# Performance work log

Measured on AMD Instinct MI355X. Metric: run time of the kernel, lower is better.

The kernel has to match this reference:

```python
import jax, jax.numpy as jnp
import numpy as np

N_NODES = 100000
N_EDGES = 1600000
IN_DIM = 128
HID_DIM = 128
OUT_DIM = 64
NUM_GRAPHS = 64


def setup_inputs() -> dict:
    key = jax.random.key(0)
    k = jax.random.split(key, 8)
    x = jax.random.normal(k[0], (N_NODES, IN_DIM), dtype=jnp.float32)
    edge_index = jax.random.randint(k[1], (2, N_EDGES), 0, N_NODES, dtype=jnp.int64)
    batch = jnp.sort(jax.random.randint(k[2], (N_NODES,), 0, NUM_GRAPHS, dtype=jnp.int64))
    # glorot-ish init for GCN weights, zero bias (PyG default)
    W1 = jax.random.normal(k[3], (IN_DIM, HID_DIM), dtype=jnp.float32) / np.sqrt(IN_DIM)
    b1 = jnp.zeros((HID_DIM,), dtype=jnp.float32)
    W2 = jax.random.normal(k[4], (HID_DIM, OUT_DIM), dtype=jnp.float32) / np.sqrt(HID_DIM)
    b2 = jnp.zeros((OUT_DIM,), dtype=jnp.float32)
    return {"x": x, "edge_index": edge_index, "batch": batch,
            "W1": W1, "b1": b1, "W2": W2, "b2": b2}


def _gcn_conv(x, W, b, src, dst, norm, n_nodes):
    # x' = scatter_add_{dst}(norm * (xW)[src]) + b   (self-loops already in src/dst)
    h = x @ W                              # [N, D_out]
    msg = norm[:, None] * h[src]           # [E+N, D_out] gather + scale
    out = jax.ops.segment_sum(msg, dst, num_segments=n_nodes)
    return out + b


def _gcn_norm(src, dst, n_nodes):
    # symmetric normalization with self-loops: deg^-1/2[src] * deg^-1/2[dst]
    deg = jax.ops.segment_sum(jnp.ones_like(dst, dtype=jnp.float32), dst,
                              num_segments=n_nodes)
    dinv = jnp.where(deg > 0, jax.lax.rsqrt(deg), 0.0)
    return dinv[src] * dinv[dst]


def reference(x, edge_index, batch, W1, b1, W2, b2):
    n = x.shape[0]
    loops = jnp.arange(n, dtype=edge_index.dtype)
    src = jnp.concatenate([edge_index[0], loops])
    dst = jnp.concatenate([edge_index[1], loops])
    norm = _gcn_norm(src, dst, n)

    h = jax.nn.relu(_gcn_conv(x, W1, b1, src, dst, norm, n))
    h = jax.nn.relu(_gcn_conv(h, W2, b2, src, dst, norm, n))

    # global mean pool per graph
    sums = jax.ops.segment_sum(h, batch, num_segments=NUM_GRAPHS)
    cnts = jax.ops.segment_sum(jnp.ones((n,), dtype=h.dtype), batch,
                               num_segments=NUM_GRAPHS)
    return sums / jnp.maximum(cnts, 1.0)[:, None]
```

## Files before the change

kernel.cpp:

```cpp
#include <hip/hip_runtime.h>

typedef unsigned short ushort_t;
typedef unsigned int uint_t;
typedef __attribute__((ext_vector_type(8))) short bf16x8;
typedef __attribute__((ext_vector_type(4))) float f32x4;

__device__ inline ushort_t bf16_rne(float f) {
    uint_t u = __float_as_uint(f);
    return (ushort_t)((u + 0x7FFFu + ((u >> 16) & 1u)) >> 16);
}

__device__ inline uint_t pack2(float lo, float hi) {
    return (uint_t)bf16_rne(lo) | ((uint_t)bf16_rne(hi) << 16);
}

__device__ inline void acc8(uint4 v, float* a) {
    a[0] += __uint_as_float(v.x << 16);
    a[1] += __uint_as_float(v.x & 0xFFFF0000u);
    a[2] += __uint_as_float(v.y << 16);
    a[3] += __uint_as_float(v.y & 0xFFFF0000u);
    a[4] += __uint_as_float(v.z << 16);
    a[5] += __uint_as_float(v.z & 0xFFFF0000u);
    a[6] += __uint_as_float(v.w << 16);
    a[7] += __uint_as_float(v.w & 0xFFFF0000u);
}

__device__ inline void set8(uint4 v, float* a) {
    a[0] = __uint_as_float(v.x << 16);
    a[1] = __uint_as_float(v.x & 0xFFFF0000u);
    a[2] = __uint_as_float(v.y << 16);
    a[3] = __uint_as_float(v.y & 0xFFFF0000u);
    a[4] = __uint_as_float(v.z << 16);
    a[5] = __uint_as_float(v.z & 0xFFFF0000u);
    a[6] = __uint_as_float(v.w << 16);
    a[7] = __uint_as_float(v.w & 0xFFFF0000u);
}


#define BSH 8
#define NBMAX 512
#define EPB 4096

__global__ __launch_bounds__(256) void k_bhist(const int* __restrict__ dst,
                                               int* __restrict__ bcnt, int E, int nb) {
    __shared__ int h[NBMAX];
    const int tid = threadIdx.x;
    for (int i = tid; i < NBMAX; i += 256) h[i] = 0;
    __syncthreads();
    const int e0 = blockIdx.x * EPB;
    for (int i = tid; i < EPB; i += 256) {
        int e = e0 + i;
        if (e < E) atomicAdd(&h[dst[e] >> BSH], 1);
    }
    __syncthreads();
    for (int i = tid; i < nb; i += 256)
        if (h[i]) atomicAdd(&bcnt[i], h[i]);
}

__global__ __launch_bounds__(512) void k_bscan(const int* __restrict__ bcnt,
                                               int* __restrict__ boff,
                                               int* __restrict__ bcur, int nb) {
    __shared__ int a[NBMAX];
    const int t = threadIdx.x;
    int v = (t < nb) ? bcnt[t] : 0;
    a[t] = v;
    __syncthreads();
    for (int off = 1; off < NBMAX; off <<= 1) {
        int x = (t >= off) ? a[t - off] : 0;
        __syncthreads();
        a[t] += x;
        __syncthreads();
    }
    if (t < nb) {
        int excl = a[t] - v;
        boff[t] = excl;
        bcur[t] = excl;
    }
}

__global__ __launch_bounds__(256) void k_bscatter(const int* __restrict__ src,
                                                  const int* __restrict__ dst,
                                                  int* __restrict__ bcur,
                                                  int2* __restrict__ pairs, int E, int nb) {
    __shared__ int h[NBMAX];
    __shared__ int base[NBMAX];
    const int tid = threadIdx.x;
    for (int i = tid; i < NBMAX; i += 256) h[i] = 0;
    __syncthreads();
    const int e0 = blockIdx.x * EPB;
    for (int i = tid; i < EPB; i += 256) {
        int e = e0 + i;
        if (e < E) atomicAdd(&h[dst[e] >> BSH], 1);
    }
    __syncthreads();
    for (int b = tid; b < nb; b += 256) {
        int c = h[b];
        base[b] = c ? atomicAdd(&bcur[b], c) : 0;
        h[b] = 0;
    }
    __syncthreads();
    for (int i = tid; i < EPB; i += 256) {
        int e = e0 + i;
        if (e < E) {
            int s = src[e], d = dst[e];
            int bk = d >> BSH;
            int off = atomicAdd(&h[bk], 1);
            pairs[base[bk] + off] = make_int2(s, d);
        }
    }
}

__global__ __launch_bounds__(256) void k_bcsr(const int2* __restrict__ pairs,
                                              const int* __restrict__ boff,
                                              const int* __restrict__ bcurEnd,
                                              int* __restrict__ rowptr,
                                              int* __restrict__ rowend,
                                              float* __restrict__ dinv,
                                              int* __restrict__ csr, int n) {
    __shared__ int deg[256], sc[256], cur[256];
    const int t = threadIdx.x;
    const int b = blockIdx.x;
    const int beg = boff[b], end = bcurEnd[b];
    deg[t] = 0;
    __syncthreads();
    for (int i = beg + t; i < end; i += 256) {
        int2 p = pairs[i];
        atomicAdd(&deg[p.y & 255], 1);
    }
    __syncthreads();
    int dv = deg[t];
    sc[t] = dv;
    __syncthreads();
    for (int off = 1; off < 256; off <<= 1) {
        int x = (t >= off) ? sc[t - off] : 0;
        __syncthreads();
        sc[t] += x;
        __syncthreads();
    }
    int excl = sc[t] - dv;
    cur[t] = excl;
    int d = (b << BSH) + t;
    if (d < n) {
        int r = beg + excl;
        rowptr[d] = r;
        rowend[d] = r + dv;
        dinv[d] = rsqrtf((float)dv + 1.0f);
    }
    __syncthreads();
    for (int i = beg + t; i < end; i += 256) {
        int2 p = pairs[i];
        int off = atomicAdd(&cur[p.y & 255], 1);
        csr[beg + off] = p.x;
    }
}


__global__ __launch_bounds__(256) void k_prep_w(const float* __restrict__ W1,
                                                const float* __restrict__ W2,
                                                ushort_t* __restrict__ Wt1,
                                                ushort_t* __restrict__ Wt2) {
    int idx = blockIdx.x * 256 + threadIdx.x;
    if (idx < 16384) {
        int k = idx >> 7, c = idx & 127;
        Wt1[c * 128 + k] = bf16_rne(W1[idx]);
    } else if (idx < 24576) {
        int j = idx - 16384;
        int k = j >> 6, c = j & 63;
        Wt2[c * 128 + k] = bf16_rne(W2[j]);
    }
}


__global__ __launch_bounds__(256) void k_gemm1(const float* __restrict__ X,
                                               const ushort_t* __restrict__ Wt,
                                               const float* __restrict__ dinv,
                                               ushort_t* __restrict__ G, int n) {
    constexpr int KP = 136;
    constexpr int NW = 64, NT = 4;
    __shared__ ushort_t Xs[128 * KP];
    __shared__ ushort_t Ws[128 * KP];

    const int tid = threadIdx.x;
    const int row0 = blockIdx.x * 128;

#pragma unroll
    for (int i = 0; i < 16; i++) {
        int idx = tid * 4 + i * 1024;
        int r = idx >> 7, k = idx & 127;
        int gr = row0 + r;
        float4 v = make_float4(0.f, 0.f, 0.f, 0.f);
        if (gr < n) v = *(const float4*)&X[(size_t)gr * 128 + k];
        ushort4 o;
        o.x = bf16_rne(v.x); o.y = bf16_rne(v.y);
        o.z = bf16_rne(v.z); o.w = bf16_rne(v.w);
        *(ushort4*)&Xs[r * KP + k] = o;
    }
#pragma unroll
    for (int i = 0; i < 8; i++) {
        int idx = tid * 8 + i * 2048;
        int r = idx >> 7, k = idx & 127;
        *(uint4*)&Ws[r * KP + k] = *(const uint4*)&Wt[idx];
    }
    __syncthreads();

    const int lane = tid & 63;
    const int wid = tid >> 6;
    const int wm = wid & 1, wn = wid >> 1;
    const int lr = lane & 15, kg = lane >> 4;

    f32x4 acc[4][NT];
#pragma unroll
    for (int mi = 0; mi < 4; mi++)
#pragma unroll
        for (int ni = 0; ni < NT; ni++)
#pragma unroll
            for (int q = 0; q < 4; q++) acc[mi][ni][q] = 0.f;

    const ushort_t* xb = &Xs[(wm * 64 + lr) * KP + kg * 8];
    const ushort_t* wb = &Ws[(wn * NW + lr) * KP + kg * 8];

#pragma unroll
    for (int ks = 0; ks < 4; ks++) {
        bf16x8 a[4], b[NT];
#pragma unroll
        for (int mi = 0; mi < 4; mi++)
            a[mi] = *(const bf16x8*)&xb[mi * 16 * KP + ks * 32];
#pragma unroll
        for (int ni = 0; ni < NT; ni++)
            b[ni] = *(const bf16x8*)&wb[ni * 16 * KP + ks * 32];
#pragma unroll
        for (int mi = 0; mi < 4; mi++)
#pragma unroll
            for (int ni = 0; ni < NT; ni++)
                acc[mi][ni] = __builtin_amdgcn_mfma_f32_16x16x32_bf16(
                    a[mi], b[ni], acc[mi][ni], 0, 0, 0);
    }

#pragma unroll
    for (int mi = 0; mi < 4; mi++) {
        int r0 = row0 + wm * 64 + mi * 16 + kg * 4;
#pragma unroll
        for (int r = 0; r < 4; r++) {
            int gr = r0 + r;
            if (gr < n) {
                float s = dinv[gr];
#pragma unroll
                for (int ni = 0; ni < NT; ni++) {
                    int c = wn * NW + ni * 16 + lr;
                    G[(size_t)gr * 128 + c] = bf16_rne(s * acc[mi][ni][r]);
                }
            }
        }
    }
}


__global__ __launch_bounds__(256) void k_gather_gemm2(const int* __restrict__ rowptr,
                                                      const int* __restrict__ rowend,
                                                      const int* __restrict__ csr,
                                                      const ushort_t* __restrict__ G1,
                                                      const float* __restrict__ dinv,
                                                      const float* __restrict__ b1,
                                                      const ushort_t* __restrict__ Wt2,
                                                      ushort_t* __restrict__ G2, int n) {
    constexpr int KP = 136;
    __shared__ ushort_t Xs[128 * KP];
    __shared__ ushort_t Ws[64 * KP];

    const int tid = threadIdx.x;
    const int row0 = blockIdx.x * 128;

#pragma unroll
    for (int i = 0; i < 4; i++) {
        int idx = tid * 8 + i * 2048;
        int r = idx >> 7, k = idx & 127;
        *(uint4*)&Ws[r * KP + k] = *(const uint4*)&Wt2[idx];
    }

    const int grp = tid >> 4;
    const int lane = tid & 15;
    const int koff = lane * 8;
    for (int it = 0; it < 8; it++) {
        int r = grp + it * 16;
        int g = row0 + r;
        uint4 ov = make_uint4(0u, 0u, 0u, 0u);
        if (g < n) {
            float a[8];
            set8(*(const uint4*)&G1[(size_t)g * 128 + koff], a);
            int e = rowptr[g];
            const int end = rowend[g];
            for (; e + 3 < end; e += 4) {
                int s0 = csr[e], s1 = csr[e + 1], s2 = csr[e + 2], s3 = csr[e + 3];
                uint4 v0 = *(const uint4*)&G1[(size_t)s0 * 128 + koff];
                uint4 v1 = *(const uint4*)&G1[(size_t)s1 * 128 + koff];
                uint4 v2 = *(const uint4*)&G1[(size_t)s2 * 128 + koff];
                uint4 v3 = *(const uint4*)&G1[(size_t)s3 * 128 + koff];
                acc8(v0, a); acc8(v1, a); acc8(v2, a); acc8(v3, a);
            }
            for (; e < end; e++) {
                int s0 = csr[e];
                acc8(*(const uint4*)&G1[(size_t)s0 * 128 + koff], a);
            }
            const float di = dinv[g];
            float4 bb0 = *(const float4*)&b1[koff];
            float4 bb1 = *(const float4*)&b1[koff + 4];
            ov.x = pack2(fmaxf(di * a[0] + bb0.x, 0.f), fmaxf(di * a[1] + bb0.y, 0.f));
            ov.y = pack2(fmaxf(di * a[2] + bb0.z, 0.f), fmaxf(di * a[3] + bb0.w, 0.f));
            ov.z = pack2(fmaxf(di * a[4] + bb1.x, 0.f), fmaxf(di * a[5] + bb1.y, 0.f));
            ov.w = pack2(fmaxf(di * a[6] + bb1.z, 0.f), fmaxf(di * a[7] + bb1.w, 0.f));
        }
        *(uint4*)&Xs[r * KP + koff] = ov;
    }
    __syncthreads();

    const int lane64 = tid & 63;
    const int wid = tid >> 6;
    const int wm = wid & 1, wn = wid >> 1;
    const int lr = lane64 & 15, kg = lane64 >> 4;

    f32x4 acc[4][2];
#pragma unroll
    for (int mi = 0; mi < 4; mi++)
#pragma unroll
        for (int ni = 0; ni < 2; ni++)
#pragma unroll
            for (int q = 0; q < 4; q++) acc[mi][ni][q] = 0.f;

    const ushort_t* xb = &Xs[(wm * 64 + lr) * KP + kg * 8];
    const ushort_t* wb = &Ws[(wn * 32 + lr) * KP + kg * 8];

#pragma unroll
    for (int ks = 0; ks < 4; ks++) {
        bf16x8 a[4], b[2];
#pragma unroll
        for (int mi = 0; mi < 4; mi++)
            a[mi] = *(const bf16x8*)&xb[mi * 16 * KP + ks * 32];
#pragma unroll
        for (int ni = 0; ni < 2; ni++)
            b[ni] = *(const bf16x8*)&wb[ni * 16 * KP + ks * 32];
#pragma unroll
        for (int mi = 0; mi < 4; mi++)
#pragma unroll
            for (int ni = 0; ni < 2; ni++)
                acc[mi][ni] = __builtin_amdgcn_mfma_f32_16x16x32_bf16(
                    a[mi], b[ni], acc[mi][ni], 0, 0, 0);
    }

#pragma unroll
    for (int mi = 0; mi < 4; mi++) {
        int r0 = row0 + wm * 64 + mi * 16 + kg * 4;
#pragma unroll
        for (int r = 0; r < 4; r++) {
            int gr = r0 + r;
            if (gr < n) {
                float s = dinv[gr];
#pragma unroll
                for (int ni = 0; ni < 2; ni++) {
                    int c = wn * 32 + ni * 16 + lr;
                    G2[(size_t)gr * 64 + c] = bf16_rne(s * acc[mi][ni][r]);
                }
            }
        }
    }
}


__global__ __launch_bounds__(256) void k_gather64_pool(const int* __restrict__ rowptr,
                                                       const int* __restrict__ rowend,
                                                       const int* __restrict__ csr,
                                                       const ushort_t* __restrict__ G,
                                                       const float* __restrict__ dinv,
                                                       const float* __restrict__ b,
                                                       const int* __restrict__ batch,
                                                       float* __restrict__ pool, int n) {
    __shared__ float po[32][72];
    __shared__ int pg[32];
    const int grp = threadIdx.x >> 3;
    const int lane = threadIdx.x & 7;
    const int g = blockIdx.x * 32 + grp;
    const int koff = lane * 8;

    float o8[8] = {0.f, 0.f, 0.f, 0.f, 0.f, 0.f, 0.f, 0.f};
    if (g < n) {
        float a[8];
        set8(*(const uint4*)&G[(size_t)g * 64 + koff], a);
        int e = rowptr[g];
        const int end = rowend[g];
        for (; e + 3 < end; e += 4) {
            int s0 = csr[e], s1 = csr[e + 1], s2 = csr[e + 2], s3 = csr[e + 3];
            uint4 v0 = *(const uint4*)&G[(size_t)s0 * 64 + koff];
            uint4 v1 = *(const uint4*)&G[(size_t)s1 * 64 + koff];
            uint4 v2 = *(const uint4*)&G[(size_t)s2 * 64 + koff];
            uint4 v3 = *(const uint4*)&G[(size_t)s3 * 64 + koff];
            acc8(v0, a); acc8(v1, a); acc8(v2, a); acc8(v3, a);
        }
        for (; e < end; e++) {
            int s0 = csr[e];
            acc8(*(const uint4*)&G[(size_t)s0 * 64 + koff], a);
        }
        const float di = dinv[g];
        float4 bb0 = *(const float4*)&b[koff];
        float4 bb1 = *(const float4*)&b[koff + 4];
        o8[0] = fmaxf(di * a[0] + bb0.x, 0.f);
        o8[1] = fmaxf(di * a[1] + bb0.y, 0.f);
        o8[2] = fmaxf(di * a[2] + bb0.z, 0.f);
        o8[3] = fmaxf(di * a[3] + bb0.w, 0.f);
        o8[4] = fmaxf(di * a[4] + bb1.x, 0.f);
        o8[5] = fmaxf(di * a[5] + bb1.y, 0.f);
        o8[6] = fmaxf(di * a[6] + bb1.z, 0.f);
        o8[7] = fmaxf(di * a[7] + bb1.w, 0.f);
    }
    if (lane == 0) pg[grp] = (g < n) ? batch[g] : -1;
    *(float4*)&po[grp][koff] = make_float4(o8[0], o8[1], o8[2], o8[3]);
    *(float4*)&po[grp][koff + 4] = make_float4(o8[4], o8[5], o8[6], o8[7]);
    __syncthreads();

    if (threadIdx.x < 64) {
        const int c = threadIdx.x;
        float run = 0.f;
        int cur = -1;
        for (int r = 0; r < 32; r++) {
            int gr = pg[r];
            if (gr < 0) continue;
            if (gr != cur) {
                if (cur >= 0) atomicAdd(&pool[cur * 64 + c], run);
                cur = gr;
                run = 0.f;
            }
            run += po[r][c];
        }
        if (cur >= 0) atomicAdd(&pool[cur * 64 + c], run);
    }
}


__global__ __launch_bounds__(64) void k_div_bs(const float* __restrict__ pool,
                                               const int* __restrict__ batch,
                                               float* __restrict__ out, int n) {
    int t = blockIdx.x * 64 + threadIdx.x;
    int g = t >> 6;
    int lo = 0, hi = n;
    while (lo < hi) { int m = (lo + hi) >> 1; if (batch[m] < g) lo = m + 1; else hi = m; }
    int lb = lo;
    lo = lb; hi = n;
    while (lo < hi) { int m = (lo + hi) >> 1; if (batch[m] <= g) lo = m + 1; else hi = m; }
    float c = (float)(lo - lb);
    c = c > 1.f ? c : 1.f;
    out[t] = pool[t] / c;
}


extern "C" void kernel_launch(void* const* d_in, const int* in_sizes, int n_in,
                              void* d_out, int out_size, void* d_ws, size_t ws_size,
                              hipStream_t stream) {
    const float* x = (const float*)d_in[0];
    const int* edge = (const int*)d_in[1];
    const int* batch = (const int*)d_in[2];
    const float* W1 = (const float*)d_in[3];
    const float* b1 = (const float*)d_in[4];
    const float* W2 = (const float*)d_in[5];
    const float* b2 = (const float*)d_in[6];

    const int n = in_sizes[0] / 128;
    const int E = in_sizes[1] / 2;
    const int* src = edge;
    const int* dst = edge + E;
    const int nb = (n + 255) >> BSH;

    size_t nA = ((size_t)n + 255) & ~(size_t)255;
    float* dinv = (float*)d_ws;
    int* rowptr = (int*)(dinv + nA);
    int* rowend = rowptr + nA;
    int* bcnt = rowend + nA;
    int* boff = bcnt + NBMAX;
    int* bcur = boff + NBMAX;
    float* pool = (float*)(bcur + NBMAX);
    ushort_t* Wt1 = (ushort_t*)(pool + 4096 + 256);
    ushort_t* Wt2 = Wt1 + 16384;
    ushort_t* bufG1 = Wt2 + 8192;
    ushort_t* bufG2 = bufG1 + (size_t)n * 128;
    int* csr = (int*)(bufG2 + (size_t)n * 64);
    int2* pairs = (int2*)bufG1;

    hipMemsetAsync(bcnt, 0, NBMAX * 4, stream);
    hipMemsetAsync(pool, 0, 4096 * 4, stream);

    k_prep_w<<<96, 256, 0, stream>>>(W1, W2, Wt1, Wt2);

    int gE = (E + EPB - 1) / EPB;
    k_bhist<<<gE, 256, 0, stream>>>(dst, bcnt, E, nb);
    k_bscan<<<1, NBMAX, 0, stream>>>(bcnt, boff, bcur, nb);
    k_bscatter<<<gE, 256, 0, stream>>>(src, dst, bcur, pairs, E, nb);
    k_bcsr<<<nb, 256, 0, stream>>>(pairs, boff, bcur, rowptr, rowend, dinv, csr, n);

    k_gemm1<<<(n + 127) / 128, 256, 0, stream>>>(x, Wt1, dinv, bufG1, n);

    k_gather_gemm2<<<(n + 127) / 128, 256, 0, stream>>>(rowptr, rowend, csr, bufG1,
                                                        dinv, b1, Wt2, bufG2, n);

    k_gather64_pool<<<(n + 31) / 32, 256, 0, stream>>>(rowptr, rowend, csr, bufG2,
                                                       dinv, b2, batch, pool, n);

    k_div_bs<<<64, 64, 0, stream>>>(pool, batch, (float*)d_out, n);
}
```

Before: 243.2 us.

## Split layer-1 features into 16-column channel planes for cache-friendly gathers

The first GEMM now writes its output as eight 16-column channel planes of 32 bytes per node. The layer-1 gather runs as a separate grid over (node block, channel), so each pass touches a plane small enough to stay resident in L2/LLC. Its result goes to a new H buffer, and a standalone GEMM2 reads H back. The layer-2 gather switches to 16 threads per node with 8-byte loads and 8-way unrolling. The cost is an extra kernel launch, a full round trip of H through memory, and eight reads of the CSR index list.

```diff
diff --git a/kernel.cpp b/kernel.cpp
--- a/kernel.cpp
+++ b/kernel.cpp
@@ -34,6 +34,15 @@
     a[5] = __uint_as_float(v.z & 0xFFFF0000u);
     a[6] = __uint_as_float(v.w << 16);
     a[7] = __uint_as_float(v.w & 0xFFFF0000u);
+}
+
+__device__ inline float4 bf4_to_f4(uint2 v) {
+    float4 f;
+    f.x = __uint_as_float(v.x << 16);
+    f.y = __uint_as_float(v.x & 0xFFFF0000u);
+    f.z = __uint_as_float(v.y << 16);
+    f.w = __uint_as_float(v.y & 0xFFFF0000u);
+    return f;
 }
 
 
@@ -176,12 +185,12 @@
                                                const float* __restrict__ dinv,
                                                ushort_t* __restrict__ G, int n) {
     constexpr int KP = 136;
-    constexpr int NW = 64, NT = 4;
     __shared__ ushort_t Xs[128 * KP];
     __shared__ ushort_t Ws[128 * KP];
 
     const int tid = threadIdx.x;
     const int row0 = blockIdx.x * 128;
+    const size_t n16 = (size_t)n * 16;
 
 #pragma unroll
     for (int i = 0; i < 16; i++) {
@@ -208,30 +217,30 @@
     const int wm = wid & 1, wn = wid >> 1;
     const int lr = lane & 15, kg = lane >> 4;
 
-    f32x4 acc[4][NT];
+    f32x4 acc[4][4];
 #pragma unroll
     for (int mi = 0; mi < 4; mi++)
 #pragma unroll
-        for (int ni = 0; ni < NT; ni++)
+        for (int ni = 0; ni < 4; ni++)
 #pragma unroll
             for (int q = 0; q < 4; q++) acc[mi][ni][q] = 0.f;
 
     const ushort_t* xb = &Xs[(wm * 64 + lr) * KP + kg * 8];
-    const ushort_t* wb = &Ws[(wn * NW + lr) * KP + kg * 8];
+    const ushort_t* wb = &Ws[(wn * 64 + lr) * KP + kg * 8];
 
 #pragma unroll
     for (int ks = 0; ks < 4; ks++) {
-        bf16x8 a[4], b[NT];
+        bf16x8 a[4], b[4];
 #pragma unroll
         for (int mi = 0; mi < 4; mi++)
             a[mi] = *(const bf16x8*)&xb[mi * 16 * KP + ks * 32];
 #pragma unroll
-        for (int ni = 0; ni < NT; ni++)
+        for (int ni = 0; ni < 4; ni++)
             b[ni] = *(const bf16x8*)&wb[ni * 16 * KP + ks * 32];
 #pragma unroll
         for (int mi = 0; mi < 4; mi++)
 #pragma unroll
-            for (int ni = 0; ni < NT; ni++)
+            for (int ni = 0; ni < 4; ni++)
                 acc[mi][ni] = __builtin_amdgcn_mfma_f32_16x16x32_bf16(
                     a[mi], b[ni], acc[mi][ni], 0, 0, 0);
     }
@@ -245,9 +254,10 @@
             if (gr < n) {
                 float s = dinv[gr];
 #pragma unroll
-                for (int ni = 0; ni < NT; ni++) {
-                    int c = wn * NW + ni * 16 + lr;
-                    G[(size_t)gr * 128 + c] = bf16_rne(s * acc[mi][ni][r]);
+                for (int ni = 0; ni < 4; ni++) {
+                    int ch = wn * 4 + ni;
+                    G[(size_t)ch * n16 + (size_t)gr * 16 + lr] =
+                        bf16_rne(s * acc[mi][ni][r]);
                 }
             }
         }
@@ -255,68 +265,83 @@
 }
 
 
-__global__ __launch_bounds__(256) void k_gather_gemm2(const int* __restrict__ rowptr,
-                                                      const int* __restrict__ rowend,
-                                                      const int* __restrict__ csr,
-                                                      const ushort_t* __restrict__ G1,
-                                                      const float* __restrict__ dinv,
-                                                      const float* __restrict__ b1,
-                                                      const ushort_t* __restrict__ Wt2,
-                                                      ushort_t* __restrict__ G2, int n) {
+__global__ __launch_bounds__(256) void k_gather128c(const int* __restrict__ rowptr,
+                                                    const int* __restrict__ rowend,
+                                                    const int* __restrict__ csr,
+                                                    const ushort_t* __restrict__ G1,
+                                                    const float* __restrict__ dinv,
+                                                    const float* __restrict__ b1,
+                                                    ushort_t* __restrict__ H, int n) {
+    const int ch = blockIdx.y;
+    const int g = blockIdx.x * 128 + (threadIdx.x >> 1);
+    const int off = (threadIdx.x & 1) * 8;
+    if (g >= n) return;
+    const size_t n16 = (size_t)n * 16;
+    const ushort_t* Gc = G1 + (size_t)ch * n16;
+
+    float a[8];
+    set8(*(const uint4*)&Gc[(size_t)g * 16 + off], a);
+    int e = rowptr[g];
+    const int end = rowend[g];
+    for (; e + 3 < end; e += 4) {
+        int s0 = csr[e], s1 = csr[e + 1], s2 = csr[e + 2], s3 = csr[e + 3];
+        uint4 v0 = *(const uint4*)&Gc[(size_t)s0 * 16 + off];
+        uint4 v1 = *(const uint4*)&Gc[(size_t)s1 * 16 + off];
+        uint4 v2 = *(const uint4*)&Gc[(size_t)s2 * 16 + off];
+        uint4 v3 = *(const uint4*)&Gc[(size_t)s3 * 16 + off];
+        acc8(v0, a); acc8(v1, a); acc8(v2, a); acc8(v3, a);
+    }
+    for (; e < end; e++) {
+        int s0 = csr[e];
+        acc8(*(const uint4*)&Gc[(size_t)s0 * 16 + off], a);
+    }
+    const float di = dinv[g];
+    float4 bb0 = *(const float4*)&b1[ch * 16 + off];
+    float4 bb1 = *(const float4*)&b1[ch * 16 + off + 4];
+    uint4 ov;
+    ov.x = pack2(fmaxf(di * a[0] + bb0.x, 0.f), fmaxf(di * a[1] + bb0.y, 0.f));
+    ov.y = pack2(fmaxf(di * a[2] + bb0.z, 0.f), fmaxf(di * a[3] + bb0.w, 0.f));
+    ov.z = pack2(fmaxf(di * a[4] + bb1.x, 0.f), fmaxf(di * a[5] + bb1.y, 0.f));
+    ov.w = pack2(fmaxf(di * a[6] + bb1.z, 0.f), fmaxf(di * a[7] + bb1.w, 0.f));
+    *(uint4*)&H[(size_t)ch * n16 + (size_t)g * 16 + off] = ov;
+}
+
+
+__global__ __launch_bounds__(256) void k_gemm2(const ushort_t* __restrict__ H,
+                                               const ushort_t* __restrict__ Wt,
+                                               const float* __restrict__ dinv,
+                                               ushort_t* __restrict__ G2, int n) {
     constexpr int KP = 136;
     __shared__ ushort_t Xs[128 * KP];
     __shared__ ushort_t Ws[64 * KP];
 
     const int tid = threadIdx.x;
     const int row0 = blockIdx.x * 128;
-
+    const size_t n16 = (size_t)n * 16;
+
+#pragma unroll
+    for (int i = 0; i < 8; i++) {
+        int u = tid + i * 256;
+        int ch = u >> 8;
+        int rr = (u & 255) >> 1;
+        int hh = (u & 1) * 8;
+        int gr = row0 + rr;
+        uint4 v = make_uint4(0u, 0u, 0u, 0u);
+        if (gr < n) v = *(const uint4*)&H[(size_t)ch * n16 + (size_t)gr * 16 + hh];
+        *(uint4*)&Xs[rr * KP + ch * 16 + hh] = v;
+    }
 #pragma unroll
     for (int i = 0; i < 4; i++) {
         int idx = tid * 8 + i * 2048;
         int r = idx >> 7, k = idx & 127;
-        *(uint4*)&Ws[r * KP + k] = *(const uint4*)&Wt2[idx];
-    }
-
-    const int grp = tid >> 4;
-    const int lane = tid & 15;
-    const int koff = lane * 8;
-    for (int it = 0; it < 8; it++) {
-        int r = grp + it * 16;
-        int g = row0 + r;
-        uint4 ov = make_uint4(0u, 0u, 0u, 0u);
-        if (g < n) {
-            float a[8];
-            set8(*(const uint4*)&G1[(size_t)g * 128 + koff], a);
-            int e = rowptr[g];
-            const int end = rowend[g];
-            for (; e + 3 < end; e += 4) {
-                int s0 = csr[e], s1 = csr[e + 1], s2 = csr[e + 2], s3 = csr[e + 3];
-                uint4 v0 = *(const uint4*)&G1[(size_t)s0 * 128 + koff];
-                uint4 v1 = *(const uint4*)&G1[(size_t)s1 * 128 + koff];
-                uint4 v2 = *(const uint4*)&G1[(size_t)s2 * 128 + koff];
-                uint4 v3 = *(const uint4*)&G1[(size_t)s3 * 128 + koff];
-                acc8(v0, a); acc8(v1, a); acc8(v2, a); acc8(v3, a);
-            }
-            for (; e < end; e++) {
-                int s0 = csr[e];
-                acc8(*(const uint4*)&G1[(size_t)s0 * 128 + koff], a);
-            }
-            const float di = dinv[g];
-            float4 bb0 = *(const float4*)&b1[koff];
-            float4 bb1 = *(const float4*)&b1[koff + 4];
-            ov.x = pack2(fmaxf(di * a[0] + bb0.x, 0.f), fmaxf(di * a[1] + bb0.y, 0.f));
-            ov.y = pack2(fmaxf(di * a[2] + bb0.z, 0.f), fmaxf(di * a[3] + bb0.w, 0.f));
-            ov.z = pack2(fmaxf(di * a[4] + bb1.x, 0.f), fmaxf(di * a[5] + bb1.y, 0.f));
-            ov.w = pack2(fmaxf(di * a[6] + bb1.z, 0.f), fmaxf(di * a[7] + bb1.w, 0.f));
-        }
-        *(uint4*)&Xs[r * KP + koff] = ov;
-    }
-    __syncthreads();
-
-    const int lane64 = tid & 63;
+        *(uint4*)&Ws[r * KP + k] = *(const uint4*)&Wt[idx];
+    }
+    __syncthreads();
+
+    const int lane = tid & 63;
     const int wid = tid >> 6;
     const int wm = wid & 1, wn = wid >> 1;
-    const int lr = lane64 & 15, kg = lane64 >> 4;
+    const int lr = lane & 15, kg = lane >> 4;
 
     f32x4 acc[4][2];
 #pragma unroll
@@ -373,53 +398,60 @@
                                                        const float* __restrict__ b,
                                                        const int* __restrict__ batch,
                                                        float* __restrict__ pool, int n) {
-    __shared__ float po[32][72];
-    __shared__ int pg[32];
-    const int grp = threadIdx.x >> 3;
-    const int lane = threadIdx.x & 7;
-    const int g = blockIdx.x * 32 + grp;
-    const int koff = lane * 8;
-
-    float o8[8] = {0.f, 0.f, 0.f, 0.f, 0.f, 0.f, 0.f, 0.f};
+    __shared__ float po[16][68];
+    __shared__ int pg[16];
+    const int grp = threadIdx.x / 16;
+    const int lane = threadIdx.x & 15;
+    const int g = blockIdx.x * 16 + grp;
+
+    float4 o = make_float4(0.f, 0.f, 0.f, 0.f);
     if (g < n) {
-        float a[8];
-        set8(*(const uint4*)&G[(size_t)g * 64 + koff], a);
-        int e = rowptr[g];
-        const int end = rowend[g];
-        for (; e + 3 < end; e += 4) {
-            int s0 = csr[e], s1 = csr[e + 1], s2 = csr[e + 2], s3 = csr[e + 3];
-            uint4 v0 = *(const uint4*)&G[(size_t)s0 * 64 + koff];
-            uint4 v1 = *(const uint4*)&G[(size_t)s1 * 64 + koff];
-            uint4 v2 = *(const uint4*)&G[(size_t)s2 * 64 + koff];
-            uint4 v3 = *(const uint4*)&G[(size_t)s3 * 64 + koff];
-            acc8(v0, a); acc8(v1, a); acc8(v2, a); acc8(v3, a);
-        }
-        for (; e < end; e++) {
+        const int beg = rowptr[g], end = rowend[g];
+        float4 acc = bf4_to_f4(*(const uint2*)&G[(size_t)g * 64 + lane * 4]);
+        int e = beg;
+        for (; e + 7 < end; e += 8) {
+            int s[8];
+#pragma unroll
+            for (int j = 0; j < 8; j++) s[j] = csr[e + j];
+            uint2 rr[8];
+#pragma unroll
+            for (int j = 0; j < 8; j++)
+                rr[j] = *(const uint2*)&G[(size_t)s[j] * 64 + lane * 4];
+#pragma unroll
+            for (int j = 0; j < 8; j++) {
+                float4 a = bf4_to_f4(rr[j]);
+                acc.x += a.x; acc.y += a.y; acc.z += a.z; acc.w += a.w;
+            }
+        }
+        for (; e + 1 < end; e += 2) {
+            int s0 = csr[e], s1 = csr[e + 1];
+            uint2 r0 = *(const uint2*)&G[(size_t)s0 * 64 + lane * 4];
+            uint2 r1 = *(const uint2*)&G[(size_t)s1 * 64 + lane * 4];
+            float4 a0 = bf4_to_f4(r0), a1 = bf4_to_f4(r1);
+            acc.x += a0.x + a1.x; acc.y += a0.y + a1.y;
+            acc.z += a0.z + a1.z; acc.w += a0.w + a1.w;
+        }
+        if (e < end) {
             int s0 = csr[e];
-            acc8(*(const uint4*)&G[(size_t)s0 * 64 + koff], a);
+            float4 a = bf4_to_f4(*(const uint2*)&G[(size_t)s0 * 64 + lane * 4]);
+            acc.x += a.x; acc.y += a.y; acc.z += a.z; acc.w += a.w;
         }
         const float di = dinv[g];
-        float4 bb0 = *(const float4*)&b[koff];
-        float4 bb1 = *(const float4*)&b[koff + 4];
-        o8[0] = fmaxf(di * a[0] + bb0.x, 0.f);
-        o8[1] = fmaxf(di * a[1] + bb0.y, 0.f);
-        o8[2] = fmaxf(di * a[2] + bb0.z, 0.f);
-        o8[3] = fmaxf(di * a[3] + bb0.w, 0.f);
-        o8[4] = fmaxf(di * a[4] + bb1.x, 0.f);
-        o8[5] = fmaxf(di * a[5] + bb1.y, 0.f);
-        o8[6] = fmaxf(di * a[6] + bb1.z, 0.f);
-        o8[7] = fmaxf(di * a[7] + bb1.w, 0.f);
+        float4 bb = *(const float4*)&b[lane * 4];
+        o.x = fmaxf(di * acc.x + bb.x, 0.f);
+        o.y = fmaxf(di * acc.y + bb.y, 0.f);
+        o.z = fmaxf(di * acc.z + bb.z, 0.f);
+        o.w = fmaxf(di * acc.w + bb.w, 0.f);
     }
     if (lane == 0) pg[grp] = (g < n) ? batch[g] : -1;
-    *(float4*)&po[grp][koff] = make_float4(o8[0], o8[1], o8[2], o8[3]);
-    *(float4*)&po[grp][koff + 4] = make_float4(o8[4], o8[5], o8[6], o8[7]);
+    *(float4*)&po[grp][lane * 4] = o;
     __syncthreads();
 
     if (threadIdx.x < 64) {
         const int c = threadIdx.x;
         float run = 0.f;
         int cur = -1;
-        for (int r = 0; r < 32; r++) {
+        for (int r = 0; r < 16; r++) {
             int gr = pg[r];
             if (gr < 0) continue;
             if (gr != cur) {
@@ -477,10 +509,10 @@
     float* pool = (float*)(bcur + NBMAX);
     ushort_t* Wt1 = (ushort_t*)(pool + 4096 + 256);
     ushort_t* Wt2 = Wt1 + 16384;
-    ushort_t* bufG1 = Wt2 + 8192;
-    ushort_t* bufG2 = bufG1 + (size_t)n * 128;
-    int* csr = (int*)(bufG2 + (size_t)n * 64);
-    int2* pairs = (int2*)bufG1;
+    ushort_t* bufG = Wt2 + 8192;
+    ushort_t* bufH = bufG + (size_t)n * 128;
+    int* csr = (int*)(bufH + (size_t)n * 128);
+    int2* pairs = (int2*)bufG;
 
     hipMemsetAsync(bcnt, 0, NBMAX * 4, stream);
     hipMemsetAsync(pool, 0, 4096 * 4, stream);
@@ -493,13 +525,15 @@
     k_bscatter<<<gE, 256, 0, stream>>>(src, dst, bcur, pairs, E, nb);
     k_bcsr<<<nb, 256, 0, stream>>>(pairs, boff, bcur, rowptr, rowend, dinv, csr, n);
 
-    k_gemm1<<<(n + 127) / 128, 256, 0, stream>>>(x, Wt1, dinv, bufG1, n);
-
-    k_gather_gemm2<<<(n + 127) / 128, 256, 0, stream>>>(rowptr, rowend, csr, bufG1,
-                                                        dinv, b1, Wt2, bufG2, n);
-
-    k_gather64_pool<<<(n + 31) / 32, 256, 0, stream>>>(rowptr, rowend, csr, bufG2,
-                                                       dinv, b2, batch, pool, n);
+    k_gemm1<<<(n + 127) / 128, 256, 0, stream>>>(x, Wt1, dinv, bufG, n);
+
+    int nbx = (((n + 127) / 128) + 7) & ~7;
+    k_gather128c<<<dim3(nbx, 8), 256, 0, stream>>>(rowptr, rowend, csr, bufG, dinv, b1,
+                                                   bufH, n);
+
+    k_gemm2<<<(n + 127) / 128, 256, 0, stream>>>(bufH, Wt2, dinv, bufG, n);
+    k_gather64_pool<<<(n + 15) / 16, 256, 0, stream>>>(rowptr, rowend, csr, bufG, dinv,
+                                                       b2, batch, pool, n);
 
     k_div_bs<<<64, 64, 0, stream>>>(pool, batch, (float*)d_out, n);
 }
```

Result: slower. 272.8 us (+12.1%).
